# Kernel tuning notes

Measured on AMD Instinct MI355X. Metric: run time of the kernel, lower is better.

Reference implementation:

```python
import jax, jax.numpy as jnp
import numpy as np

DIM = 1024
HEADS = 16
DIM_HEAD = 64
INNER = HEADS * DIM_HEAD  # 1024
FF_INNER = 4 * DIM        # 4096
EPS = 1e-5


def _ln(t, gamma):
    mu = jnp.mean(t, axis=-1, keepdims=True)
    var = jnp.var(t, axis=-1, keepdims=True)
    return (t - mu) * jax.lax.rsqrt(var + EPS) * gamma


def setup_inputs() -> dict:
    key = jax.random.key(0)
    ks = jax.random.split(key, 8)
    B, N = 4, 1024
    s = 0.02
    return {
        "x": jax.random.normal(ks[0], (B, N, DIM), dtype=jnp.float32),
        "y": jax.random.normal(ks[1], (B, N, DIM), dtype=jnp.float32),
        "g1": jnp.ones((DIM,), dtype=jnp.float32),
        "g2": jnp.ones((DIM,), dtype=jnp.float32),
        "g_out": jnp.ones((DIM,), dtype=jnp.float32),
        "Wq": jax.random.normal(ks[2], (DIM, INNER), dtype=jnp.float32) * s,
        "Wkv": jax.random.normal(ks[3], (DIM, 2 * DIM_HEAD), dtype=jnp.float32) * s,
        "Wo": jax.random.normal(ks[4], (INNER, DIM), dtype=jnp.float32) * s,
        "Wff1": jax.random.normal(ks[5], (DIM, 2 * FF_INNER), dtype=jnp.float32) * s,
        "Wff2": jax.random.normal(ks[6], (FF_INNER, DIM), dtype=jnp.float32) * s,
    }


def reference(x, y, g1, g2, g_out, Wq, Wkv, Wo, Wff1, Wff2):
    B, N, _ = x.shape
    scale = DIM_HEAD ** -0.5
    xn = _ln(x, g1)
    yn = _ln(y, g2)  # note: torch code rebinds y = norm2(y); residual & FF use normed y
    # multi-query attention: per-head queries, single shared k/v head
    q = (xn @ Wq).reshape(B, N, HEADS, DIM_HEAD).transpose(0, 2, 1, 3) * scale  # b h n d
    kv = yn @ Wkv  # b j (2d)
    k, v = kv[..., :DIM_HEAD], kv[..., DIM_HEAD:]
    sim = jnp.einsum('bhid,bjd->bhij', q, k)
    attn = jax.nn.softmax(sim, axis=-1)  # torch code subtracts amax then softmax; identical math
    out = jnp.einsum('bhij,bjd->bhid', attn, v)
    out = out.transpose(0, 2, 1, 3).reshape(B, N, INNER)
    out = out @ Wo
    out = _ln(out + yn, g_out)
    # SwiGLU FFN on normed y: first half is value, second half is gate
    h = yn @ Wff1
    val, gate = h[..., :FF_INNER], h[..., FF_INNER:]
    ff = (jax.nn.silu(gate) * val) @ Wff2
    return out + ff
```

## Files before the change

kernel.cpp:

```cpp
#include <hip/hip_runtime.h>
#include <hip/hip_bf16.h>


typedef __attribute__((ext_vector_type(8))) short bf16x8;
typedef __attribute__((ext_vector_type(4))) short s16x4;
typedef __attribute__((ext_vector_type(4))) float f32x4;

__device__ __forceinline__ short f2b(float f) {
  union { float f; unsigned u; } v; v.f = f;
  unsigned r = (v.u + 0x7fffu + ((v.u >> 16) & 1u)) >> 16;
  return (short)r;
}

__device__ __forceinline__ void gload16(const short* g, short* l) {
  __builtin_amdgcn_global_load_lds(
      (const __attribute__((address_space(1))) void*)g,
      (__attribute__((address_space(3))) void*)l, 16, 0, 0);
}

__global__ __launch_bounds__(256) void cvtT_kernel(const float* __restrict__ in,
                                                   short* __restrict__ out,
                                                   int K, int N) {
  __shared__ float tile[32][33];
  int n0 = blockIdx.x * 32, k0 = blockIdx.y * 32;
  int tx = threadIdx.x & 7, ty = threadIdx.x >> 3;
  float4 v = *(const float4*)&in[(size_t)(k0 + ty) * N + n0 + tx * 4];
  tile[ty][tx * 4 + 0] = v.x;
  tile[ty][tx * 4 + 1] = v.y;
  tile[ty][tx * 4 + 2] = v.z;
  tile[ty][tx * 4 + 3] = v.w;
  __syncthreads();
  s16x4 o = { f2b(tile[tx * 4 + 0][ty]), f2b(tile[tx * 4 + 1][ty]),
              f2b(tile[tx * 4 + 2][ty]), f2b(tile[tx * 4 + 3][ty]) };
  *(s16x4*)&out[(size_t)(n0 + ty) * K + k0 + tx * 4] = o;
}

__global__ __launch_bounds__(256) void ln_kernel(const float* __restrict__ in,
                                                 const float* __restrict__ gamma,
                                                 short* __restrict__ out16,
                                                 float* __restrict__ out32) {
  int row = blockIdx.x;
  int t = threadIdx.x;
  float4 v = ((const float4*)(in + (size_t)row * 1024))[t];
  float s  = v.x + v.y + v.z + v.w;
  float sq = v.x*v.x + v.y*v.y + v.z*v.z + v.w*v.w;
  __shared__ float ssum[256], ssq[256];
  ssum[t] = s; ssq[t] = sq;
  __syncthreads();
  for (int o = 128; o > 0; o >>= 1) {
    if (t < o) { ssum[t] += ssum[t + o]; ssq[t] += ssq[t + o]; }
    __syncthreads();
  }
  float mu  = ssum[0] * (1.0f / 1024.0f);
  float var = ssq[0] * (1.0f / 1024.0f) - mu * mu;
  float rs  = rsqrtf(var + 1e-5f);
  float4 g = ((const float4*)gamma)[t];
  float o0 = (v.x - mu) * rs * g.x;
  float o1 = (v.y - mu) * rs * g.y;
  float o2 = (v.z - mu) * rs * g.z;
  float o3 = (v.w - mu) * rs * g.w;
  if (out16) {
    s16x4 o = { f2b(o0), f2b(o1), f2b(o2), f2b(o3) };
    ((s16x4*)out16)[(size_t)row * 256 + t] = o;
  }
  if (out32) {
    float4 o = { o0, o1, o2, o3 };
    ((float4*)out32)[(size_t)row * 256 + t] = o;
  }
}

template<int EPI, int BM, int BN>
__global__ __launch_bounds__(256, 2) void gemm_ring(
    const short* __restrict__ A, const short* __restrict__ B,
    int M, int N, int Kstride, int Klen,
    short* __restrict__ out16, float* __restrict__ out32,
    const float* __restrict__ res, float scale)
{
  constexpr int DEPTH = 4;
  constexpr int FM = BM / 32;
  constexpr int FN = BN / 32;
  constexpr int AL = BM / 64;
  constexpr int BL = BN / 64;
  __shared__ __align__(16) short As[DEPTH][BM * 32];
  __shared__ __align__(16) short Bs[DEPTH][BN * 32];

  int t = threadIdx.x;
  int lane = t & 63, wave = t >> 6;
  int wm = wave >> 1, wn = wave & 1;
  int lrow = lane & 15, lgrp = lane >> 4;
  int m0 = blockIdx.y * BM, n0 = blockIdx.x * BN;
  int kbase = blockIdx.z * Klen;

  int srow = lane >> 2, scol = (lane & 3) * 8;
  const short* gA = A + (size_t)(m0 + wave * 16 + srow) * Kstride + kbase + scol;
  const short* gB = B + (size_t)(n0 + wave * 16 + srow) * Kstride + kbase + scol;

  auto STAGE = [&](int slot, int kt) {
    int k0 = kt * 32;
#pragma unroll
    for (int i = 0; i < AL; i++)
      gload16(gA + (size_t)(i * 64) * Kstride + k0, &As[slot][(i * 4 + wave) * 512]);
#pragma unroll
    for (int j = 0; j < BL; j++)
      gload16(gB + (size_t)(j * 64) * Kstride + k0, &Bs[slot][(j * 4 + wave) * 512]);
  };

  f32x4 acc[FM][FN];
  const f32x4 zero = { 0.f, 0.f, 0.f, 0.f };
#pragma unroll
  for (int i = 0; i < FM; i++)
#pragma unroll
    for (int j = 0; j < FN; j++) acc[i][j] = zero;

  int nt = Klen / 32;
#pragma unroll
  for (int p = 0; p < DEPTH - 1; p++) STAGE(p, p);

  int slot = 0, stage_slot = DEPTH - 1;
  for (int tI = 0; tI < nt; ++tI) {
    int rem = nt - 1 - tI;
    if constexpr (AL + BL == 4) {
      if (rem >= 2)      asm volatile("s_waitcnt vmcnt(8)" ::: "memory");
      else if (rem == 1) asm volatile("s_waitcnt vmcnt(4)" ::: "memory");
      else               asm volatile("s_waitcnt vmcnt(0)" ::: "memory");
    } else {
      if (rem >= 2)      asm volatile("s_waitcnt vmcnt(6)" ::: "memory");
      else if (rem == 1) asm volatile("s_waitcnt vmcnt(3)" ::: "memory");
      else               asm volatile("s_waitcnt vmcnt(0)" ::: "memory");
    }
    __builtin_amdgcn_s_barrier();
    __builtin_amdgcn_sched_barrier(0);

    if (tI + DEPTH - 1 < nt) STAGE(stage_slot, tI + DEPTH - 1);

    bf16x8 af[FM], bfr[FN];
#pragma unroll
    for (int mf = 0; mf < FM; mf++)
      af[mf] = *(const bf16x8*)&As[slot][(wm * (BM / 2) + mf * 16 + lrow) * 32 + lgrp * 8];
#pragma unroll
    for (int nf = 0; nf < FN; nf++)
      bfr[nf] = *(const bf16x8*)&Bs[slot][(wn * (BN / 2) + nf * 16 + lrow) * 32 + lgrp * 8];

    __builtin_amdgcn_s_setprio(1);
#pragma unroll
    for (int mf = 0; mf < FM; mf++)
#pragma unroll
      for (int nf = 0; nf < FN; nf++)
        acc[mf][nf] = __builtin_amdgcn_mfma_f32_16x16x32_bf16(af[mf], bfr[nf], acc[mf][nf], 0, 0, 0);
    __builtin_amdgcn_s_setprio(0);

    slot = (slot + 1 == DEPTH) ? 0 : slot + 1;
    stage_slot = (stage_slot + 1 == DEPTH) ? 0 : stage_slot + 1;
  }

#pragma unroll
  for (int mf = 0; mf < FM; mf++)
#pragma unroll
    for (int nf = 0; nf < FN; nf++)
#pragma unroll
      for (int r = 0; r < 4; r++) {
        int row = m0 + wm * (BM / 2) + mf * 16 + lgrp * 4 + r;
        int col = n0 + wn * (BN / 2) + nf * 16 + lrow;
        float v = acc[mf][nf][r];
        if (EPI == 0) {
          out16[(size_t)row * N + col] = f2b(v * scale);
        } else if (EPI == 1) {
          out32[(size_t)row * N + col] = v + res[(size_t)row * N + col];
        } else {
          out32[(size_t)blockIdx.z * M * N + (size_t)row * N + col] = v;
        }
      }
}

__global__ __launch_bounds__(512, 2) void gemm_ff1(
    const short* __restrict__ A, const short* __restrict__ B,
    short* __restrict__ out16)
{
  constexpr int K = 1024, NT = 16;
  __shared__ __align__(16) short As[2][256 * 64];
  __shared__ __align__(16) short Bv[2][128 * 64];
  __shared__ __align__(16) short Bg[2][128 * 64];

  int t = threadIdx.x;
  int lane = t & 63, wave = t >> 6;
  int wm = wave >> 2, wn = wave & 3;
  int lrow = lane & 15, lgrp = lane >> 4;
  int m0 = blockIdx.y * 256, n0 = blockIdx.x * 128;

  int srow8 = lane >> 3;
  int schunk = ((lane & 7) ^ srow8) * 8;
  const short* gA  = A + (size_t)(m0 + wave * 8 + srow8) * K + schunk;
  const short* gBv = B + (size_t)(n0 + wave * 8 + srow8) * K + schunk;
  const short* gBg = B + (size_t)(4096 + n0 + wave * 8 + srow8) * K + schunk;

  f32x4 acc[8][2], acc2[8][2];
  const f32x4 zero = { 0.f, 0.f, 0.f, 0.f };
#pragma unroll
  for (int i = 0; i < 8; i++) {
    acc[i][0] = zero; acc[i][1] = zero; acc2[i][0] = zero; acc2[i][1] = zero;
  }

  int rc0 = ((lgrp) ^ (lrow & 7)) * 8;
  int rc1 = ((4 | lgrp) ^ (lrow & 7)) * 8;

#pragma unroll
  for (int i = 0; i < 4; i++)
    gload16(gA + (size_t)(i * 64) * K, &As[0][(i * 64 + wave * 8) * 64]);
#pragma unroll
  for (int j = 0; j < 2; j++) {
    gload16(gBv + (size_t)(j * 64) * K, &Bv[0][(j * 64 + wave * 8) * 64]);
    gload16(gBg + (size_t)(j * 64) * K, &Bg[0][(j * 64 + wave * 8) * 64]);
  }
  asm volatile("s_waitcnt vmcnt(0)" ::: "memory");
  __builtin_amdgcn_s_barrier();
  __builtin_amdgcn_sched_barrier(0);

  for (int tI = 0; tI < NT; ++tI) {
    int cur = tI & 1, nxt = cur ^ 1;
    bool pf = (tI + 1 < NT);
    int kn = (tI + 1) * 64;
    bf16x8 af0[8], af1[8], bvf[2], bgf[2];

#pragma unroll
    for (int mf = 0; mf < 8; mf++)
      af0[mf] = *(const bf16x8*)&As[cur][(wm * 128 + mf * 16 + lrow) * 64 + rc0];
    bvf[0] = *(const bf16x8*)&Bv[cur][(wn * 32 + lrow) * 64 + rc0];
    bvf[1] = *(const bf16x8*)&Bv[cur][(wn * 32 + 16 + lrow) * 64 + rc0];
    if (pf) {
      gload16(gA + kn,                     &As[nxt][(wave * 8) * 64]);
      gload16(gA + (size_t)64 * K + kn,    &As[nxt][(64 + wave * 8) * 64]);
      gload16(gA + (size_t)128 * K + kn,   &As[nxt][(128 + wave * 8) * 64]);
    }
    __builtin_amdgcn_s_barrier();
    asm volatile("s_waitcnt lgkmcnt(0)" ::: "memory");
    __builtin_amdgcn_sched_barrier(0);
    __builtin_amdgcn_s_setprio(1);
#pragma unroll
    for (int mf = 0; mf < 8; mf++) {
      acc[mf][0] = __builtin_amdgcn_mfma_f32_16x16x32_bf16(af0[mf], bvf[0], acc[mf][0], 0, 0, 0);
      acc[mf][1] = __builtin_amdgcn_mfma_f32_16x16x32_bf16(af0[mf], bvf[1], acc[mf][1], 0, 0, 0);
    }
    __builtin_amdgcn_s_setprio(0);
    __builtin_amdgcn_s_barrier();
    __builtin_amdgcn_sched_barrier(0);

#pragma unroll
    for (int mf = 0; mf < 8; mf++)
      af1[mf] = *(const bf16x8*)&As[cur][(wm * 128 + mf * 16 + lrow) * 64 + rc1];
    bvf[0] = *(const bf16x8*)&Bv[cur][(wn * 32 + lrow) * 64 + rc1];
    bvf[1] = *(const bf16x8*)&Bv[cur][(wn * 32 + 16 + lrow) * 64 + rc1];
    if (pf) {
      gload16(gA + (size_t)192 * K + kn,   &As[nxt][(192 + wave * 8) * 64]);
      gload16(gBv + kn,                    &Bv[nxt][(wave * 8) * 64]);
      gload16(gBv + (size_t)64 * K + kn,   &Bv[nxt][(64 + wave * 8) * 64]);
    }
    __builtin_amdgcn_s_barrier();
    asm volatile("s_waitcnt lgkmcnt(0)" ::: "memory");
    __builtin_amdgcn_sched_barrier(0);
    __builtin_amdgcn_s_setprio(1);
#pragma unroll
    for (int mf = 0; mf < 8; mf++) {
      acc[mf][0] = __builtin_amdgcn_mfma_f32_16x16x32_bf16(af1[mf], bvf[0], acc[mf][0], 0, 0, 0);
      acc[mf][1] = __builtin_amdgcn_mfma_f32_16x16x32_bf16(af1[mf], bvf[1], acc[mf][1], 0, 0, 0);
    }
    __builtin_amdgcn_s_setprio(0);
    __builtin_amdgcn_s_barrier();
    __builtin_amdgcn_sched_barrier(0);

    bgf[0] = *(const bf16x8*)&Bg[cur][(wn * 32 + lrow) * 64 + rc0];
    bgf[1] = *(const bf16x8*)&Bg[cur][(wn * 32 + 16 + lrow) * 64 + rc0];
    if (pf) {
      gload16(gBg + kn,                    &Bg[nxt][(wave * 8) * 64]);
      gload16(gBg + (size_t)64 * K + kn,   &Bg[nxt][(64 + wave * 8) * 64]);
    }
    __builtin_amdgcn_s_barrier();
    asm volatile("s_waitcnt lgkmcnt(0)" ::: "memory");
    __builtin_amdgcn_sched_barrier(0);
    __builtin_amdgcn_s_setprio(1);
#pragma unroll
    for (int mf = 0; mf < 8; mf++) {
      acc2[mf][0] = __builtin_amdgcn_mfma_f32_16x16x32_bf16(af0[mf], bgf[0], acc2[mf][0], 0, 0, 0);
      acc2[mf][1] = __builtin_amdgcn_mfma_f32_16x16x32_bf16(af0[mf], bgf[1], acc2[mf][1], 0, 0, 0);
    }
    __builtin_amdgcn_s_setprio(0);
    __builtin_amdgcn_s_barrier();
    __builtin_amdgcn_sched_barrier(0);

    bgf[0] = *(const bf16x8*)&Bg[cur][(wn * 32 + lrow) * 64 + rc1];
    bgf[1] = *(const bf16x8*)&Bg[cur][(wn * 32 + 16 + lrow) * 64 + rc1];
    __builtin_amdgcn_s_barrier();
    asm volatile("s_waitcnt lgkmcnt(0)" ::: "memory");
    __builtin_amdgcn_sched_barrier(0);
    __builtin_amdgcn_s_setprio(1);
#pragma unroll
    for (int mf = 0; mf < 8; mf++) {
      acc2[mf][0] = __builtin_amdgcn_mfma_f32_16x16x32_bf16(af1[mf], bgf[0], acc2[mf][0], 0, 0, 0);
      acc2[mf][1] = __builtin_amdgcn_mfma_f32_16x16x32_bf16(af1[mf], bgf[1], acc2[mf][1], 0, 0, 0);
    }
    __builtin_amdgcn_s_setprio(0);
    __builtin_amdgcn_s_barrier();
    __builtin_amdgcn_sched_barrier(0);

    asm volatile("s_waitcnt vmcnt(0)" ::: "memory");
    __builtin_amdgcn_s_barrier();
    __builtin_amdgcn_sched_barrier(0);
  }

#pragma unroll
  for (int mf = 0; mf < 8; mf++)
#pragma unroll
    for (int nf = 0; nf < 2; nf++)
#pragma unroll
      for (int r = 0; r < 4; r++) {
        int row = m0 + wm * 128 + mf * 16 + lgrp * 4 + r;
        int col = n0 + wn * 32 + nf * 16 + lrow;
        float v = acc[mf][nf][r];
        float gate = acc2[mf][nf][r];
        float sig = 1.0f / (1.0f + __expf(-gate));
        out16[(size_t)row * 4096 + col] = f2b(v * gate * sig);
      }
}

__global__ __launch_bounds__(256) void kvred_kernel(const float* __restrict__ p,
                                                    short* __restrict__ out, int n4) {
  int i = blockIdx.x * 256 + threadIdx.x;
  if (i >= n4) return;
  const int S = 4096 * 128 / 4;
  float4 a = ((const float4*)p)[i];
  float4 b = ((const float4*)p)[i + S];
  float4 c = ((const float4*)p)[i + 2 * S];
  float4 d = ((const float4*)p)[i + 3 * S];
  s16x4 o = { f2b(a.x + b.x + c.x + d.x), f2b(a.y + b.y + c.y + d.y),
              f2b(a.z + b.z + c.z + d.z), f2b(a.w + b.w + c.w + d.w) };
  ((s16x4*)out)[i] = o;
}

__global__ __launch_bounds__(256) void attn_kernel(const short* __restrict__ q,
                                                   const short* __restrict__ kv,
                                                   short* __restrict__ ao)
{
  __shared__ __align__(16) short Ks[64 * 64];
  __shared__ __align__(16) short Vs[64 * 64];
  __shared__ __align__(16) short Ps[4][32 * 64];

  int t = threadIdx.x;
  int lane = t & 63, wave = t >> 6;
  int lrow = lane & 15, lgrp = lane >> 4;
  int qt = blockIdx.x;
  int b = blockIdx.y >> 2, hg = blockIdx.y & 3;
  int h = hg * 4 + wave;

  char* Kb = (char*)Ks;
  char* Vb = (char*)Vs;
  char* Pb = (char*)Ps + wave * (32 * 64 * 2);

  bf16x8 qf[2][2];
  const short* qb = q + ((size_t)(b * 1024 + qt * 32)) * 1024 + h * 64;
#pragma unroll
  for (int mf = 0; mf < 2; mf++)
#pragma unroll
    for (int kk = 0; kk < 2; kk++)
      qf[mf][kk] = *(const bf16x8*)&qb[(size_t)(mf * 16 + lrow) * 1024 + kk * 32 + lgrp * 8];

  f32x4 oacc[2][4];
  float m_[2][4], l_[2][4];
  const f32x4 zero = { 0.f, 0.f, 0.f, 0.f };
#pragma unroll
  for (int i = 0; i < 2; i++)
#pragma unroll
    for (int j = 0; j < 4; j++) { oacc[i][j] = zero; }
#pragma unroll
  for (int i = 0; i < 2; i++)
#pragma unroll
    for (int r = 0; r < 4; r++) { m_[i][r] = -3.0e38f; l_[i][r] = 0.f; }

  int4 d[4];
  {
    const short* kvb = kv + ((size_t)(b * 1024 + lane)) * 128 + wave * 32;
#pragma unroll
    for (int i = 0; i < 4; i++) d[i] = ((const int4*)kvb)[i];
  }

  for (int j0 = 0; j0 < 1024; j0 += 64) {
    __builtin_amdgcn_s_barrier();
    __builtin_amdgcn_sched_barrier(0);
    asm volatile("s_waitcnt vmcnt(0)" ::: "memory");
    if (wave < 2) {
      int sw = (lane & 7) << 4;
#pragma unroll
      for (int i = 0; i < 4; i++)
        *(int4*)(Kb + lane * 128 + ((wave * 64 + i * 16) ^ sw)) = d[i];
    } else {
#pragma unroll
      for (int i = 0; i < 4; i++) {
        union { int4 v; short s[8]; } u; u.v = d[i];
#pragma unroll
        for (int j = 0; j < 8; j++) {
          int dd = (wave - 2) * 32 + i * 8 + j;
          *(short*)(Vb + dd * 128 + ((lane * 2) ^ ((dd & 7) << 4))) = u.s[j];
        }
      }
    }
    if (j0 + 64 < 1024) {
      const short* kvn = kv + ((size_t)(b * 1024 + j0 + 64 + lane)) * 128 + wave * 32;
#pragma unroll
      for (int i = 0; i < 4; i++) d[i] = ((const int4*)kvn)[i];
    }
    asm volatile("s_waitcnt lgkmcnt(0)" ::: "memory");
    __builtin_amdgcn_s_barrier();
    __builtin_amdgcn_sched_barrier(0);

    bf16x8 kf[4][2];
#pragma unroll
    for (int nf = 0; nf < 4; nf++) {
      int row = nf * 16 + lrow, sw = (row & 7) << 4;
      kf[nf][0] = *(const bf16x8*)(Kb + row * 128 + ((lgrp * 16) ^ sw));
      kf[nf][1] = *(const bf16x8*)(Kb + row * 128 + ((64 + lgrp * 16) ^ sw));
    }
    f32x4 sacc[2][4];
#pragma unroll
    for (int i = 0; i < 2; i++)
#pragma unroll
      for (int j = 0; j < 4; j++) sacc[i][j] = zero;
    __builtin_amdgcn_s_setprio(1);
#pragma unroll
    for (int mf = 0; mf < 2; mf++)
#pragma unroll
      for (int nf = 0; nf < 4; nf++)
#pragma unroll
        for (int kk = 0; kk < 2; kk++)
          sacc[mf][nf] = __builtin_amdgcn_mfma_f32_16x16x32_bf16(qf[mf][kk], kf[nf][kk], sacc[mf][nf], 0, 0, 0);
    __builtin_amdgcn_s_setprio(0);

    float pmax[2][4];
    bool okd = true;
#pragma unroll
    for (int mf = 0; mf < 2; mf++)
#pragma unroll
      for (int r = 0; r < 4; r++) {
        float pm = fmaxf(fmaxf(sacc[mf][0][r], sacc[mf][1][r]),
                         fmaxf(sacc[mf][2][r], sacc[mf][3][r]));
        pmax[mf][r] = pm;
        okd = okd && (pm <= m_[mf][r] + 8.0f);
      }
    if (__all(okd)) {
#pragma unroll
      for (int mf = 0; mf < 2; mf++)
#pragma unroll
        for (int r = 0; r < 4; r++) {
          int row = mf * 16 + lgrp * 4 + r, sw = (row & 7) << 4;
          float al = 0.f;
#pragma unroll
          for (int nf = 0; nf < 4; nf++) {
            float p = __expf(sacc[mf][nf][r] - m_[mf][r]);
            *(short*)(Pb + row * 128 + (((nf * 16 + lrow) * 2) ^ sw)) = f2b(p);
            al += p;
          }
          l_[mf][r] += al;
        }
    } else {
#pragma unroll
      for (int mf = 0; mf < 2; mf++)
#pragma unroll
        for (int r = 0; r < 4; r++) {
          float mx = pmax[mf][r];
#pragma unroll
          for (int o = 8; o >= 1; o >>= 1) mx = fmaxf(mx, __shfl_xor(mx, o));
          float mnew = fmaxf(m_[mf][r], mx);
          float corr = __expf(m_[mf][r] - mnew);
          int row = mf * 16 + lgrp * 4 + r, sw = (row & 7) << 4;
          float al = 0.f;
#pragma unroll
          for (int nf = 0; nf < 4; nf++) {
            float p = __expf(sacc[mf][nf][r] - mnew);
            *(short*)(Pb + row * 128 + (((nf * 16 + lrow) * 2) ^ sw)) = f2b(p);
            al += p;
          }
          l_[mf][r] = l_[mf][r] * corr + al;
          m_[mf][r] = mnew;
#pragma unroll
          for (int nf = 0; nf < 4; nf++) oacc[mf][nf][r] *= corr;
        }
    }

    bf16x8 vf[4][2], pfr[2][2];
#pragma unroll
    for (int nf = 0; nf < 4; nf++) {
      int row = nf * 16 + lrow, sw = (row & 7) << 4;
      vf[nf][0] = *(const bf16x8*)(Vb + row * 128 + ((lgrp * 16) ^ sw));
      vf[nf][1] = *(const bf16x8*)(Vb + row * 128 + ((64 + lgrp * 16) ^ sw));
    }
#pragma unroll
    for (int mf = 0; mf < 2; mf++) {
      int row = mf * 16 + lrow, sw = (row & 7) << 4;
      pfr[mf][0] = *(const bf16x8*)(Pb + row * 128 + ((lgrp * 16) ^ sw));
      pfr[mf][1] = *(const bf16x8*)(Pb + row * 128 + ((64 + lgrp * 16) ^ sw));
    }
    __builtin_amdgcn_s_setprio(1);
#pragma unroll
    for (int mf = 0; mf < 2; mf++)
#pragma unroll
      for (int nf = 0; nf < 4; nf++)
#pragma unroll
        for (int kk = 0; kk < 2; kk++)
          oacc[mf][nf] = __builtin_amdgcn_mfma_f32_16x16x32_bf16(pfr[mf][kk], vf[nf][kk], oacc[mf][nf], 0, 0, 0);
    __builtin_amdgcn_s_setprio(0);
  }

#pragma unroll
  for (int mf = 0; mf < 2; mf++)
#pragma unroll
    for (int r = 0; r < 4; r++) {
      float ls = l_[mf][r];
#pragma unroll
      for (int o = 8; o >= 1; o >>= 1) ls += __shfl_xor(ls, o);
      float inv = 1.0f / ls;
      int qrow = qt * 32 + mf * 16 + lgrp * 4 + r;
#pragma unroll
      for (int nf = 0; nf < 4; nf++) {
        float val = oacc[mf][nf][r] * inv;
        ao[((size_t)(b * 1024 + qrow)) * 1024 + h * 64 + nf * 16 + lrow] = f2b(val);
      }
    }
}

extern "C" void kernel_launch(void* const* d_in, const int* in_sizes, int n_in,
                              void* d_out, int out_size, void* d_ws, size_t ws_size,
                              hipStream_t stream) {
  const float* x     = (const float*)d_in[0];
  const float* y     = (const float*)d_in[1];
  const float* g1    = (const float*)d_in[2];
  const float* g2    = (const float*)d_in[3];
  const float* g_out = (const float*)d_in[4];
  const float* Wq    = (const float*)d_in[5];
  const float* Wkv   = (const float*)d_in[6];
  const float* Wo    = (const float*)d_in[7];
  const float* Wff1  = (const float*)d_in[8];
  const float* Wff2  = (const float*)d_in[9];

  char* ws = (char*)d_ws;
  size_t off = 0;
  auto alloc = [&](size_t bytes) { char* p = ws + off; off += bytes; return p; };
  short* wqT    = (short*)alloc((size_t)1024 * 1024 * 2);
  short* wkvT   = (short*)alloc((size_t)128 * 1024 * 2);
  short* woT    = (short*)alloc((size_t)1024 * 1024 * 2);
  short* wff1T  = (short*)alloc((size_t)8192 * 1024 * 2);
  short* wff2T  = (short*)alloc((size_t)1024 * 4096 * 2);
  short* xn16   = (short*)alloc((size_t)4096 * 1024 * 2);
  short* yn16   = (short*)alloc((size_t)4096 * 1024 * 2);
  float* ynf    = (float*)alloc((size_t)4096 * 1024 * 4);
  short* q16    = (short*)alloc((size_t)4096 * 1024 * 2);
  short* kv16   = (short*)alloc((size_t)4096 * 128 * 2);
  short* ao16   = (short*)alloc((size_t)4096 * 1024 * 2);
  float* lnout  = (float*)alloc((size_t)4096 * 1024 * 4);
  short* act16  = (short*)alloc((size_t)4096 * 4096 * 2);
  float* kvpart = (float*)alloc((size_t)4 * 4096 * 128 * 4);
  float* outf   = (float*)d_out;

  cvtT_kernel<<<dim3(1024 / 32, 1024 / 32), 256, 0, stream>>>(Wq,   wqT,   1024, 1024);
  cvtT_kernel<<<dim3(128 / 32, 1024 / 32),  256, 0, stream>>>(Wkv,  wkvT,  1024, 128);
  cvtT_kernel<<<dim3(1024 / 32, 1024 / 32), 256, 0, stream>>>(Wo,   woT,   1024, 1024);
  cvtT_kernel<<<dim3(8192 / 32, 1024 / 32), 256, 0, stream>>>(Wff1, wff1T, 1024, 8192);
  cvtT_kernel<<<dim3(1024 / 32, 4096 / 32), 256, 0, stream>>>(Wff2, wff2T, 4096, 1024);

  ln_kernel<<<4096, 256, 0, stream>>>(x, g1, xn16, nullptr);
  ln_kernel<<<4096, 256, 0, stream>>>(y, g2, yn16, ynf);

  gemm_ring<0, 64, 128><<<dim3(8, 64), 256, 0, stream>>>(
      xn16, wqT, 4096, 1024, 1024, 1024, q16, nullptr, nullptr, 0.125f);
  gemm_ring<3, 64, 128><<<dim3(1, 64, 4), 256, 0, stream>>>(
      yn16, wkvT, 4096, 128, 1024, 256, nullptr, kvpart, nullptr, 1.0f);
  kvred_kernel<<<512, 256, 0, stream>>>(kvpart, kv16, 4096 * 128 / 4);

  attn_kernel<<<dim3(32, 16), 256, 0, stream>>>(q16, kv16, ao16);

  gemm_ring<1, 64, 128><<<dim3(8, 64), 256, 0, stream>>>(
      ao16, woT, 4096, 1024, 1024, 1024, nullptr, outf, ynf, 1.0f);

  ln_kernel<<<4096, 256, 0, stream>>>(outf, g_out, nullptr, lnout);

  gemm_ff1<<<dim3(32, 16), 512, 0, stream>>>(yn16, wff1T, act16);

  gemm_ring<1, 64, 128><<<dim3(8, 64), 256, 0, stream>>>(
      act16, wff2T, 4096, 1024, 4096, 4096, nullptr, outf, lnout, 1.0f);
}
```

Measured before the change: 316.7 us.

## Pre-transpose V in kv reduction and double-buffer K/V via direct LDS loads

The kv reduction kernel now also writes a transposed copy of V to global memory. The attention kernel then stages K and V^T tiles straight into double-buffered LDS with global_load_lds, replacing the register round-trip and the scalar per-element V transpose stores. Prefetching the next tile while computing the current one is meant to hide load latency and remove the LDS transpose cost. The price is extra strided 2-byte global writes in kvred and twice the LDS for K/V.

```diff
diff --git a/kernel.cpp b/kernel.cpp
--- a/kernel.cpp
+++ b/kernel.cpp
@@ -322,9 +322,9 @@
 }
 
 __global__ __launch_bounds__(256) void kvred_kernel(const float* __restrict__ p,
-                                                    short* __restrict__ out, int n4) {
+                                                    short* __restrict__ out,
+                                                    short* __restrict__ vT) {
   int i = blockIdx.x * 256 + threadIdx.x;
-  if (i >= n4) return;
   const int S = 4096 * 128 / 4;
   float4 a = ((const float4*)p)[i];
   float4 b = ((const float4*)p)[i + S];
@@ -333,14 +333,25 @@
   s16x4 o = { f2b(a.x + b.x + c.x + d.x), f2b(a.y + b.y + c.y + d.y),
               f2b(a.z + b.z + c.z + d.z), f2b(a.w + b.w + c.w + d.w) };
   ((s16x4*)out)[i] = o;
+  int row = i >> 5, col4 = i & 31;
+  if (col4 >= 16) {
+    int bb = row >> 10, n = row & 1023;
+    int dbase = col4 * 4 - 64;
+    short* vt = vT + ((size_t)(bb * 64 + dbase)) * 1024 + n;
+    vt[0]        = o[0];
+    vt[1024]     = o[1];
+    vt[2048]     = o[2];
+    vt[3072]     = o[3];
+  }
 }
 
 __global__ __launch_bounds__(256) void attn_kernel(const short* __restrict__ q,
                                                    const short* __restrict__ kv,
+                                                   const short* __restrict__ vT,
                                                    short* __restrict__ ao)
 {
-  __shared__ __align__(16) short Ks[64 * 64];
-  __shared__ __align__(16) short Vs[64 * 64];
+  __shared__ __align__(16) short Ks[2][64 * 64];
+  __shared__ __align__(16) short Vt[2][64 * 64];
   __shared__ __align__(16) short Ps[4][32 * 64];
 
   int t = threadIdx.x;
@@ -350,9 +361,19 @@
   int b = blockIdx.y >> 2, hg = blockIdx.y & 3;
   int h = hg * 4 + wave;
 
-  char* Kb = (char*)Ks;
-  char* Vb = (char*)Vs;
   char* Pb = (char*)Ps + wave * (32 * 64 * 2);
+
+  int r8 = lane >> 3;
+  int schunk = ((lane & 7) ^ r8) * 8;
+  const short* gK = kv + ((size_t)(b * 1024 + wave * 16 + r8)) * 128 + schunk;
+  const short* gV = vT + ((size_t)(b * 64 + wave * 16 + r8)) * 1024 + schunk;
+
+  auto STAGE = [&](int buf, int j0) {
+    gload16(gK + (size_t)(j0 + 0) * 128, &Ks[buf][(wave * 16 + 0) * 64]);
+    gload16(gK + (size_t)(j0 + 8) * 128, &Ks[buf][(wave * 16 + 8) * 64]);
+    gload16(gV + j0,                     &Vt[buf][(wave * 16 + 0) * 64]);
+    gload16(gV + (size_t)8 * 1024 + j0,  &Vt[buf][(wave * 16 + 8) * 64]);
+  };
 
   bf16x8 qf[2][2];
   const short* qb = q + ((size_t)(b * 1024 + qt * 32)) * 1024 + h * 64;
@@ -374,48 +395,26 @@
 #pragma unroll
     for (int r = 0; r < 4; r++) { m_[i][r] = -3.0e38f; l_[i][r] = 0.f; }
 
-  int4 d[4];
-  {
-    const short* kvb = kv + ((size_t)(b * 1024 + lane)) * 128 + wave * 32;
-#pragma unroll
-    for (int i = 0; i < 4; i++) d[i] = ((const int4*)kvb)[i];
-  }
-
-  for (int j0 = 0; j0 < 1024; j0 += 64) {
-    __builtin_amdgcn_s_barrier();
-    __builtin_amdgcn_sched_barrier(0);
-    asm volatile("s_waitcnt vmcnt(0)" ::: "memory");
-    if (wave < 2) {
-      int sw = (lane & 7) << 4;
-#pragma unroll
-      for (int i = 0; i < 4; i++)
-        *(int4*)(Kb + lane * 128 + ((wave * 64 + i * 16) ^ sw)) = d[i];
-    } else {
-#pragma unroll
-      for (int i = 0; i < 4; i++) {
-        union { int4 v; short s[8]; } u; u.v = d[i];
-#pragma unroll
-        for (int j = 0; j < 8; j++) {
-          int dd = (wave - 2) * 32 + i * 8 + j;
-          *(short*)(Vb + dd * 128 + ((lane * 2) ^ ((dd & 7) << 4))) = u.s[j];
-        }
-      }
-    }
-    if (j0 + 64 < 1024) {
-      const short* kvn = kv + ((size_t)(b * 1024 + j0 + 64 + lane)) * 128 + wave * 32;
-#pragma unroll
-      for (int i = 0; i < 4; i++) d[i] = ((const int4*)kvn)[i];
-    }
-    asm volatile("s_waitcnt lgkmcnt(0)" ::: "memory");
+  STAGE(0, 0);
+
+  for (int tI = 0; tI < 16; ++tI) {
+    int cur = tI & 1;
+    int j0 = tI * 64;
+    __builtin_amdgcn_s_barrier();
+    __builtin_amdgcn_sched_barrier(0);
+    if (tI + 1 < 16) STAGE(cur ^ 1, j0 + 64);
+    __builtin_amdgcn_sched_barrier(0);
+    if (tI + 1 < 16) asm volatile("s_waitcnt vmcnt(4)" ::: "memory");
+    else             asm volatile("s_waitcnt vmcnt(0)" ::: "memory");
     __builtin_amdgcn_s_barrier();
     __builtin_amdgcn_sched_barrier(0);
 
     bf16x8 kf[4][2];
 #pragma unroll
     for (int nf = 0; nf < 4; nf++) {
-      int row = nf * 16 + lrow, sw = (row & 7) << 4;
-      kf[nf][0] = *(const bf16x8*)(Kb + row * 128 + ((lgrp * 16) ^ sw));
-      kf[nf][1] = *(const bf16x8*)(Kb + row * 128 + ((64 + lgrp * 16) ^ sw));
+      int row = nf * 16 + lrow;
+      kf[nf][0] = *(const bf16x8*)&Ks[cur][row * 64 + ((lgrp ^ (row & 7)) * 8)];
+      kf[nf][1] = *(const bf16x8*)&Ks[cur][row * 64 + (((4 | lgrp) ^ (row & 7)) * 8)];
     }
     f32x4 sacc[2][4];
 #pragma unroll
@@ -486,9 +485,9 @@
     bf16x8 vf[4][2], pfr[2][2];
 #pragma unroll
     for (int nf = 0; nf < 4; nf++) {
-      int row = nf * 16 + lrow, sw = (row & 7) << 4;
-      vf[nf][0] = *(const bf16x8*)(Vb + row * 128 + ((lgrp * 16) ^ sw));
-      vf[nf][1] = *(const bf16x8*)(Vb + row * 128 + ((64 + lgrp * 16) ^ sw));
+      int row = nf * 16 + lrow;
+      vf[nf][0] = *(const bf16x8*)&Vt[cur][row * 64 + ((lgrp ^ (row & 7)) * 8)];
+      vf[nf][1] = *(const bf16x8*)&Vt[cur][row * 64 + (((4 | lgrp) ^ (row & 7)) * 8)];
     }
 #pragma unroll
     for (int mf = 0; mf < 2; mf++) {
@@ -551,6 +550,7 @@
   float* ynf    = (float*)alloc((size_t)4096 * 1024 * 4);
   short* q16    = (short*)alloc((size_t)4096 * 1024 * 2);
   short* kv16   = (short*)alloc((size_t)4096 * 128 * 2);
+  short* vT16   = (short*)alloc((size_t)4 * 64 * 1024 * 2);
   short* ao16   = (short*)alloc((size_t)4096 * 1024 * 2);
   float* lnout  = (float*)alloc((size_t)4096 * 1024 * 4);
   short* act16  = (short*)alloc((size_t)4096 * 4096 * 2);
@@ -570,9 +570,9 @@
       xn16, wqT, 4096, 1024, 1024, 1024, q16, nullptr, nullptr, 0.125f);
   gemm_ring<3, 64, 128><<<dim3(1, 64, 4), 256, 0, stream>>>(
       yn16, wkvT, 4096, 128, 1024, 256, nullptr, kvpart, nullptr, 1.0f);
-  kvred_kernel<<<512, 256, 0, stream>>>(kvpart, kv16, 4096 * 128 / 4);
-
-  attn_kernel<<<dim3(32, 16), 256, 0, stream>>>(q16, kv16, ao16);
+  kvred_kernel<<<512, 256, 0, stream>>>(kvpart, kv16, vT16);
+
+  attn_kernel<<<dim3(32, 16), 256, 0, stream>>>(q16, kv16, vT16, ao16);
 
   gemm_ring<1, 64, 128><<<dim3(8, 64), 256, 0, stream>>>(
       ao16, woT, 4096, 1024, 1024, 1024, nullptr, outf, ynf, 1.0f);
```

Result: faster. 286.5 us, median of 2 (-9.5%).
